# Kernel tuning notes

Measured on AMD Instinct MI355X. Metric: run time of the kernel, lower is better.

## Reference

```python
import jax, jax.numpy as jnp
import numpy as np

NUM_AGENT = 200
LOOK_BACK = 10
NUM_CTRL = 9
DIM = 512
HEADS = 8
DIM_HEAD = 64
N = NUM_AGENT * LOOK_BACK + NUM_CTRL  # 2009
BATCH = 4
SCALE = DIM_HEAD ** -0.5


def _build_mask():
    # eye(num_agent) repeat_interleaved by look_back on rows and cols == kron with ones(lb,lb)
    m = jnp.kron(jnp.eye(NUM_AGENT, dtype=jnp.float32),
                 jnp.ones((LOOK_BACK, LOOK_BACK), jnp.float32))
    # pad with zeros for the control-feature rows/cols
    return jnp.pad(m, ((0, NUM_CTRL), (0, NUM_CTRL)))  # [N, N]


def _split_heads(t):
    b, n, hd = t.shape
    return t.reshape(b, n, HEADS, hd // HEADS).transpose(0, 2, 1, 3)  # [b,h,n,d]


def setup_inputs() -> dict:
    key = jax.random.key(0)
    ks = jax.random.split(key, 5)
    inner = HEADS * DIM_HEAD
    return {
        "x": jax.random.normal(ks[0], (BATCH, N, DIM), jnp.float32),
        "w_qkv": jax.random.normal(ks[1], (DIM, inner * 3), jnp.float32) * 0.02,
        "w_qk_self": jax.random.normal(ks[2], (DIM, inner * 2), jnp.float32) * 0.02,
        "w_out": jax.random.normal(ks[3], (inner, DIM), jnp.float32) * 0.02,
        "b_out": jnp.zeros((DIM,), jnp.float32),
    }


def reference(x, w_qkv, w_qk_self, w_out, b_out):
    mask = _build_mask()  # [N, N], broadcasts over [b, h]
    q, k, v = map(_split_heads, jnp.split(x @ w_qkv, 3, axis=-1))
    q_s, k_s = map(_split_heads, jnp.split(x @ w_qk_self, 2, axis=-1))
    dots = jnp.einsum('bhnd,bhmd->bhnm', q, k) * SCALE
    dots_self = jnp.einsum('bhnd,bhmd->bhnm', q_s, k_s) * SCALE
    blended = mask * dots_self + (1.0 - mask) * dots
    attn = jax.nn.softmax(blended, axis=-1)  # [b,h,n,n]
    out = jnp.einsum('bhnm,bhmd->bhnd', attn, v)
    out = out.transpose(0, 2, 1, 3).reshape(x.shape[0], N, HEADS * DIM_HEAD)
    return out @ w_out + b_out, attn
```

## Files before the change

### kernel.cpp

```cpp
#include <hip/hip_runtime.h>
#include <hip/hip_bf16.h>


#define N_TOK   2009
#define NPAD    2048
#define NTILES  16
#define NT2     32
#define BATCH_  4
#define HEADS_  8
#define MROWS   8036
#define SCALE_  0.125f
#define RPB_A   256
#define RPV     64
#define PFP     68

typedef __attribute__((ext_vector_type(8)))  short sh8;
typedef __attribute__((ext_vector_type(16))) float f32x16;

static inline int cdiv(int a, int b) { return (a + b - 1) / b; }

__device__ __forceinline__ float4 ld4(const float* p) {
    return *reinterpret_cast<const float4*>(p);
}
__device__ __forceinline__ unsigned short f2bf(float f) {
    __hip_bfloat16 h = __float2bfloat16(f);
    return *reinterpret_cast<unsigned short*>(&h);
}
__device__ __forceinline__ float bf2f(unsigned short u) {
    return __uint_as_float(((unsigned)u) << 16);
}
__device__ __forceinline__ void cvt8(const float4& a, const float4& b, sh8& hi, sh8& lo) {
    float f[8] = {a.x, a.y, a.z, a.w, b.x, b.y, b.z, b.w};
#pragma unroll
    for (int i = 0; i < 8; ++i) {
        unsigned short h = f2bf(f[i]);
        hi[i] = (short)h;
        lo[i] = (short)f2bf(f[i] - bf2f(h));
    }
}
__device__ __forceinline__ void cvt8p(const float4& a, const float4& b, sh8& hi) {
#pragma unroll
    for (int i = 0; i < 4; ++i) {
        hi[i]     = (short)f2bf((&a.x)[i]);
        hi[4 + i] = (short)f2bf((&b.x)[i]);
    }
}
typedef const __attribute__((address_space(1))) void gas_void;
typedef __attribute__((address_space(3))) void las_void;
__device__ __forceinline__ void gll16(const void* g, void* l) {
    __builtin_amdgcn_global_load_lds((gas_void*)g, (las_void*)l, 16, 0, 0);
}

__device__ __forceinline__ void bar_lds() {
    asm volatile("s_waitcnt lgkmcnt(0)" ::: "memory");
    __builtin_amdgcn_sched_barrier(0);
    __builtin_amdgcn_s_barrier();
    __builtin_amdgcn_sched_barrier(0);
}
__device__ __forceinline__ void bar_keep16() {
    asm volatile("s_waitcnt vmcnt(16) lgkmcnt(0)" ::: "memory");
    __builtin_amdgcn_sched_barrier(0);
    __builtin_amdgcn_s_barrier();
    __builtin_amdgcn_sched_barrier(0);
}

__global__ __launch_bounds__(256)
void convert_x(const float* __restrict__ x, unsigned short* __restrict__ xh,
               unsigned short* __restrict__ xl)
{
    const int mt = blockIdx.x;
    const int yq = blockIdx.y;
    const int w  = threadIdx.x >> 6;
    const int kc = threadIdx.x & 63;
    for (int it = 0; it < 2; ++it) {
        int rg = (yq * 2 + it) * 4 + w;
        sh8 hi[4], lo[4];
#pragma unroll
        for (int rr = 0; rr < 4; ++rr) {
            int row = rg * 4 + rr;
            int gm = mt * 128 + row;
            int b = gm >> 11, gr = gm & 2047;
            float4 a = make_float4(0.f, 0.f, 0.f, 0.f), c = a;
            if (gr < N_TOK) {
                const float* p = x + ((size_t)b * N_TOK + gr) * 512 + kc * 8;
                a = ld4(p); c = ld4(p + 4);
            }
            cvt8(a, c, hi[rr], lo[rr]);
        }
        size_t base = ((size_t)(mt * 64 + kc) * 128 + rg * 4) * 8;
#pragma unroll
        for (int rr = 0; rr < 4; ++rr) {
            *reinterpret_cast<sh8*>(xh + base + rr * 8) = hi[rr];
            *reinterpret_cast<sh8*>(xl + base + rr * 8) = lo[rr];
        }
    }
}

__global__ __launch_bounds__(256)
void convert_w(const float* __restrict__ wqkv, const float* __restrict__ wself,
               const float* __restrict__ wout,
               unsigned short* __restrict__ qh, unsigned short* __restrict__ ql,
               unsigned short* __restrict__ sh, unsigned short* __restrict__ sl,
               unsigned short* __restrict__ oh, unsigned short* __restrict__ ol)
{
    int cid = blockIdx.x * 256 + threadIdx.x;
    int nt_all = cid >> 13, rem = cid & 8191;
    int kc = rem >> 7, col = rem & 127;
    const float* src; unsigned short *dh, *dl; int Nn, ntl;
    if (nt_all < 12)      { src = wqkv;  dh = qh; dl = ql; Nn = 1536; ntl = nt_all; }
    else if (nt_all < 20) { src = wself; dh = sh; dl = sl; Nn = 1024; ntl = nt_all - 12; }
    else                  { src = wout;  dh = oh; dl = ol; Nn = 512;  ntl = nt_all - 20; }
    float f[8];
#pragma unroll
    for (int i = 0; i < 8; ++i)
        f[i] = src[(size_t)(kc * 8 + i) * Nn + ntl * 128 + col];
    sh8 hi, lo;
    cvt8(make_float4(f[0], f[1], f[2], f[3]), make_float4(f[4], f[5], f[6], f[7]), hi, lo);
    size_t off = ((size_t)(ntl * 64 + kc) * 128 + col) * 8;
    *reinterpret_cast<sh8*>(dh + off) = hi;
    *reinterpret_cast<sh8*>(dl + off) = lo;
}

template<int MODE>
__global__ __launch_bounds__(512)
void gemm_bf16(const unsigned short* __restrict__ Ah, const unsigned short* __restrict__ Al,
               const unsigned short* __restrict__ Bh, const unsigned short* __restrict__ Bl,
               float* __restrict__ C, const float* __restrict__ bias)
{
    __shared__ __align__(16) unsigned short AhS[2][4096], AlS[2][4096],
                                            BhS[2][4096], BlS[2][4096];
    const int tid = threadIdx.x, lane = tid & 63, wid = tid >> 6;
    const int mt = blockIdx.x, ntile = blockIdx.y;
    const int wm = wid >> 2, wn = wid & 3;
    const int lj = lane & 31, g = lane >> 5;

    const unsigned short* Asrc_h = Ah + (size_t)mt * 65536;
    const unsigned short* Asrc_l = Al + (size_t)mt * 65536;
    const unsigned short* Bsrc_h = Bh + (size_t)ntile * 65536;
    const unsigned short* Bsrc_l = Bl + (size_t)ntile * 65536;

#define GSTAGE(BUF, S) do {                                                      \
    gll16(Asrc_h + (size_t)(S) * 4096 + tid * 8, (char*)AhS[BUF] + tid * 16);    \
    gll16(Asrc_l + (size_t)(S) * 4096 + tid * 8, (char*)AlS[BUF] + tid * 16);    \
    gll16(Bsrc_h + (size_t)(S) * 4096 + tid * 8, (char*)BhS[BUF] + tid * 16);    \
    gll16(Bsrc_l + (size_t)(S) * 4096 + tid * 8, (char*)BlS[BUF] + tid * 16);    \
} while (0)

    f32x16 acc[2];
#pragma unroll
    for (int i = 0; i < 16; ++i) { acc[0][i] = 0.f; acc[1][i] = 0.f; }

    GSTAGE(0, 0);
    for (int s = 0; s < 16; ++s) {
        const int buf = s & 1;
        __syncthreads();
        if (s + 1 < 16) GSTAGE(buf ^ 1, s + 1);
#pragma unroll
        for (int ks = 0; ks < 2; ++ks) {
            const int kcl = 2 * ks + g;
            sh8 bh = *reinterpret_cast<const sh8*>(BhS[buf] + (kcl * 128 + wn * 32 + lj) * 8);
            sh8 bl = *reinterpret_cast<const sh8*>(BlS[buf] + (kcl * 128 + wn * 32 + lj) * 8);
#pragma unroll
            for (int Mt = 0; Mt < 2; ++Mt) {
                sh8 ah = *reinterpret_cast<const sh8*>(AhS[buf] + (kcl * 128 + wm * 64 + Mt * 32 + lj) * 8);
                sh8 al = *reinterpret_cast<const sh8*>(AlS[buf] + (kcl * 128 + wm * 64 + Mt * 32 + lj) * 8);
                acc[Mt] = __builtin_amdgcn_mfma_f32_32x32x16_bf16(ah, bh, acc[Mt], 0, 0, 0);
                acc[Mt] = __builtin_amdgcn_mfma_f32_32x32x16_bf16(ah, bl, acc[Mt], 0, 0, 0);
                acc[Mt] = __builtin_amdgcn_mfma_f32_32x32x16_bf16(al, bh, acc[Mt], 0, 0, 0);
            }
        }
    }
#undef GSTAGE

#pragma unroll
    for (int Mt = 0; Mt < 2; ++Mt) {
#pragma unroll
        for (int reg = 0; reg < 16; ++reg) {
            int rloc = wm * 64 + Mt * 32 + (reg & 3) + 8 * (reg >> 2) + 4 * g;
            int gm = mt * 128 + rloc;
            int b = gm >> 11, gr = gm & 2047;
            if (gr < N_TOK) {
                int coln = ntile * 128 + wn * 32 + lj;
                float v = acc[Mt][reg];
                size_t idx;
                if (MODE == 1)
                    idx = ((size_t)(coln >> 9) * MROWS + (size_t)b * N_TOK + gr) * 512 + (coln & 511);
                else if (MODE == 0)
                    idx = ((size_t)b * N_TOK + gr) * 1024 + coln;
                else {
                    v += bias[coln];
                    idx = ((size_t)b * N_TOK + gr) * 512 + coln;
                }
                C[idx] = v;
            }
        }
    }
}

__global__ __launch_bounds__(256)
void selfE_k(const float* __restrict__ proj2, float* __restrict__ selfE)
{
    __shared__ float qs[10][64];
    __shared__ float ks[10][68];
    const int a = blockIdx.x;
    const int h = blockIdx.y & 7;
    const int b = blockIdx.y >> 3;
    const size_t rowbase = (size_t)b * N_TOK + a * 10;

    for (int i = threadIdx.x; i < 320; i += 256) {
        int r = i >> 4;
        int c = (i & 15) * 4;
        const float* src = proj2 + (rowbase + (r % 10)) * 1024
                         + (r < 10 ? 0 : 512) + h * 64 + c;
        float4 v = ld4(src);
        if (r < 10) *reinterpret_cast<float4*>(&qs[r][c]) = v;
        else        *reinterpret_cast<float4*>(&ks[r - 10][c]) = v;
    }
    __syncthreads();
    if (threadIdx.x < 100) {
        int r = threadIdx.x / 10, c = threadIdx.x % 10;
        float acc = 0.f;
#pragma unroll 8
        for (int d = 0; d < 64; ++d) acc += qs[r][d] * ks[c][d];
        int bh = b * HEADS_ + h;
        selfE[((size_t)bh * 2000 + a * 10 + r) * 10 + c] = __expf(acc * SCALE_);
    }
}

__global__ __launch_bounds__(256)
void convert_kv(const float* __restrict__ Kf, const float* __restrict__ Vf,
                unsigned short* __restrict__ Khg, unsigned short* __restrict__ Klg,
                unsigned short* __restrict__ Vtg)
{
    __shared__ float vtile[128][66];
    const int t  = blockIdx.x;
    const int h  = blockIdx.y & 7;
    const int b  = blockIdx.y >> 3;
    const int bh = blockIdx.y;
    const size_t bN = (size_t)b * N_TOK;
    const size_t tbase = ((size_t)bh * NTILES + t) * 8192;
    const int tid = threadIdx.x;

    {
        int r = tid >> 1, q = tid & 1;
        int gj = t * 128 + r;
        float4 f[8];
        if (gj < N_TOK) {
            const float* kp = Kf + (bN + gj) * 512 + h * 64 + q * 32;
#pragma unroll
            for (int i = 0; i < 8; ++i) f[i] = ld4(kp + 4 * i);
        } else {
#pragma unroll
            for (int i = 0; i < 8; ++i) f[i] = make_float4(0.f, 0.f, 0.f, 0.f);
        }
#pragma unroll
        for (int cp = 0; cp < 4; ++cp) {
            sh8 hi, lo;
            cvt8(f[2 * cp], f[2 * cp + 1], hi, lo);
            int kc = q * 4 + cp;
            size_t off = tbase + ((size_t)kc * 128 + r) * 8;
            *reinterpret_cast<sh8*>(Khg + off) = hi;
            *reinterpret_cast<sh8*>(Klg + off) = lo;
        }
    }
    {
        int r = tid >> 1, q = tid & 1;
        int gj = t * 128 + r;
        const float* vp = Vf + (bN + gj) * 512 + h * 64 + q * 32;
#pragma unroll
        for (int i = 0; i < 8; ++i) {
            float4 v = (gj < N_TOK) ? ld4(vp + 4 * i) : make_float4(0.f, 0.f, 0.f, 0.f);
            *reinterpret_cast<float4*>(&vtile[r][q * 32 + 4 * i]) = v;
        }
    }
    __syncthreads();
    {
        int d = tid & 63, jg = tid >> 6;
#pragma unroll
        for (int jj = 0; jj < 4; ++jj) {
            int jc = jg * 4 + jj;
            sh8 pk;
#pragma unroll
            for (int i = 0; i < 8; ++i) pk[i] = (short)f2bf(vtile[jc * 8 + i][d]);
            *reinterpret_cast<sh8*>(Vtg + tbase + ((size_t)jc * 64 + d) * 8) = pk;
        }
    }
}

__global__ __launch_bounds__(512, 2)
void attn_rowsum(const float* __restrict__ Qf,
                 const unsigned short* __restrict__ Khg,
                 const float* __restrict__ selfE,
                 float* __restrict__ rowinv)
{
    __shared__ __align__(16) unsigned short KhS[2][8192];
    __shared__ float selfS[RPB_A * 10];

    const int bid = blockIdx.x;
    const int xcd = bid & 7, idx = bid >> 3;
    const int bh  = xcd * 4 + (idx >> 3);
    const int bx  = idx & 7;
    const int h = bh & 7, b = bh >> 3;
    const int tid = threadIdx.x, lane = tid & 63, wid = tid >> 6;
    const int row0 = bx * RPB_A;
    const int wr = wid * 32;
    const size_t bN = (size_t)b * N_TOK;
    const int lj = lane & 31, g = lane >> 5;

    for (int i = tid; i < RPB_A * 10; i += 512) {
        int r = i / 10, c = i - r * 10;
        int gr = row0 + r;
        selfS[i] = (gr < 2000) ? selfE[((size_t)bh * 2000 + gr) * 10 + c] : 0.f;
    }

    sh8 qh[4];
    {
        int grow = row0 + wr + lj;
        bool val = grow < N_TOK;
        const float* qp = Qf + (bN + (val ? grow : 0)) * 512 + h * 64;
#pragma unroll
        for (int ks = 0; ks < 4; ++ks) {
            int kc = 2 * ks + g;
            float4 a = val ? ld4(qp + kc * 8)     : make_float4(0.f, 0.f, 0.f, 0.f);
            float4 c = val ? ld4(qp + kc * 8 + 4) : make_float4(0.f, 0.f, 0.f, 0.f);
            cvt8p(a, c, qh[ks]);
        }
    }

    const unsigned short* ktiles = Khg + (size_t)bh * NTILES * 8192;
#define RSTAGE(T) do {                                                          \
    const unsigned short* kt = ktiles + (size_t)(T) * 8192;                     \
    char* dst = (char*)KhS[(T) & 1];                                            \
    _Pragma("unroll") for (int i = 0; i < 2; ++i)                               \
        gll16(kt + i * 4096 + tid * 8, dst + i * 8192 + tid * 16); } while (0)

    RSTAGE(0);

    float rsacc[16];
#pragma unroll
    for (int i = 0; i < 16; ++i) rsacc[i] = 0.f;

    const int alo = (row0 / 10) * 10;
    const int rmax = row0 + RPB_A - 1 < 1999 ? row0 + RPB_A - 1 : 1999;
    const int ahi = (rmax / 10) * 10 + 10;

    for (int t = 0; t < NTILES; ++t) {
        __syncthreads();
        if (t + 1 < NTILES) RSTAGE(t + 1);
        const unsigned short* kb = KhS[t & 1];
        const bool dtile = (alo < t * 128 + 128) && (ahi > t * 128);
#pragma unroll
        for (int ct = 0; ct < 4; ++ct) {
            sh8 kf[4];
#pragma unroll
            for (int ks = 0; ks < 4; ++ks)
                kf[ks] = *reinterpret_cast<const sh8*>(kb + ((2 * ks + g) * 128 + 32 * ct + lj) * 8);
            f32x16 s;
#pragma unroll
            for (int i = 0; i < 16; ++i) s[i] = 0.f;
#pragma unroll
            for (int ks = 0; ks < 4; ++ks)
                s = __builtin_amdgcn_mfma_f32_32x32x16_bf16(qh[ks], kf[ks], s, 0, 0, 0);
            const int gj = t * 128 + 32 * ct + lj;
            if (gj < N_TOK) {
#pragma unroll
                for (int reg = 0; reg < 16; ++reg) {
                    int rloc = wr + (reg & 3) + 8 * (reg >> 2) + 4 * g;
                    int grow = row0 + rloc;
                    float e = __expf(s[reg] * SCALE_);
                    if (dtile && grow < 2000) {
                        int a0 = (grow / 10) * 10;
                        unsigned cc = (unsigned)(gj - a0);
                        if (cc < 10u) e = selfS[rloc * 10 + (int)cc];
                    }
                    rsacc[reg] += e;
                }
            }
        }
    }
#undef RSTAGE

#pragma unroll
    for (int reg = 0; reg < 16; ++reg) {
        float v = rsacc[reg];
        v += __shfl_xor(v, 1);  v += __shfl_xor(v, 2);
        v += __shfl_xor(v, 4);  v += __shfl_xor(v, 8);
        v += __shfl_xor(v, 16);
        rsacc[reg] = v;
    }
    if (lj == 0) {
#pragma unroll
        for (int reg = 0; reg < 16; ++reg) {
            int rloc = wr + (reg & 3) + 8 * (reg >> 2) + 4 * g;
            int grow = row0 + rloc;
            rowinv[(size_t)bh * NPAD + row0 + rloc] =
                (grow < N_TOK) ? 1.0f / rsacc[reg] : 0.f;
        }
    }
}

__global__ __launch_bounds__(256, 3)
void attn_pv(const float* __restrict__ Qf,
             const unsigned short* __restrict__ Khg,
             const unsigned short* __restrict__ Klg,
             const unsigned short* __restrict__ Vtg,
             const float* __restrict__ selfE,
             const float* __restrict__ rowinv,
             float* __restrict__ attn,
             unsigned short* __restrict__ Ohg, unsigned short* __restrict__ Olg,
             float* __restrict__ dump)
{
    extern __shared__ __align__(16) char smem[];
    unsigned short* KhS = (unsigned short*)smem;
    unsigned short* KlS = KhS + 4096;
    unsigned short* VtS = KlS + 4096;
    float* Pf = (float*)(VtS + 8192);
    unsigned short* selfS = (unsigned short*)(Pf + RPV * PFP);
    float* rinvS = (float*)(selfS + RPV * 10);

    const int bid = blockIdx.x;
    const int xcd = bid & 7, sub = bid >> 3;
    const int bh  = xcd * 4 + (sub >> 5);
    const int bx  = sub & 31;
    const int h = bh & 7, b = bh >> 3;
    const int tid = threadIdx.x, lane = tid & 63, wid = tid >> 6;
    const int row0 = bx * RPV;
    const int wr = (wid & 1) * 32;
    const int cw = wid >> 1;
    const size_t bN = (size_t)b * N_TOK;
    const size_t abase = ((size_t)bh * N_TOK + row0) * N_TOK;
    const int lj = lane & 31, g = lane >> 5;
    float* dumpT = dump + ((size_t)bid << 6) + lane;

    for (int i = tid; i < RPV * 10; i += 256) {
        int r = i / 10, c = i - r * 10;
        int gr = row0 + r;
        selfS[i] = (gr < 2000) ? f2bf(selfE[((size_t)bh * 2000 + gr) * 10 + c]) : 0;
    }
    if (tid < RPV) rinvS[tid] = rowinv[(size_t)bh * NPAD + row0 + tid];

    sh8 qh[4], ql[4];
    {
        int grow = row0 + wr + lj;
        bool val = grow < N_TOK;
        const float* qp = Qf + (bN + (val ? grow : 0)) * 512 + h * 64;
#pragma unroll
        for (int ks = 0; ks < 4; ++ks) {
            int kc = 2 * ks + g;
            float4 a = val ? ld4(qp + kc * 8)     : make_float4(0.f, 0.f, 0.f, 0.f);
            float4 c = val ? ld4(qp + kc * 8 + 4) : make_float4(0.f, 0.f, 0.f, 0.f);
            cvt8(a, c, qh[ks], ql[ks]);
        }
    }

    const unsigned short* khT = Khg + (size_t)bh * NTILES * 8192;
    const unsigned short* klT = Klg + (size_t)bh * NTILES * 8192;
    const unsigned short* vtT = Vtg + (size_t)bh * NTILES * 8192;

#define STAGE_KH(T) do { const unsigned short* src = khT + (size_t)((T) >> 1) * 8192 \
        + 512 * ((T) & 1);                                                           \
    _Pragma("unroll") for (int r_ = 0; r_ < 2; ++r_) {                               \
        int s_ = tid + 256 * r_;                                                     \
        gll16(src + ((s_ >> 6) * 1024 + (s_ & 63) * 8), (char*)KhS + s_ * 16);       \
    } } while (0)
#define STAGE_KL(T) do { const unsigned short* src = klT + (size_t)((T) >> 1) * 8192 \
        + 512 * ((T) & 1);                                                           \
    _Pragma("unroll") for (int r_ = 0; r_ < 2; ++r_) {                               \
        int s_ = tid + 256 * r_;                                                     \
        gll16(src + ((s_ >> 6) * 1024 + (s_ & 63) * 8), (char*)KlS + s_ * 16);       \
    } } while (0)
#define STAGE_VT(T) do { const unsigned short* src = vtT + (size_t)((T) >> 1) * 8192 \
        + 4096 * ((T) & 1);                                                          \
    char* dst = (char*)VtS + ((T) & 1) * 8192;                                       \
    _Pragma("unroll") for (int r_ = 0; r_ < 2; ++r_) {                               \
        int s_ = tid + 256 * r_;                                                     \
        gll16(src + s_ * 8, dst + s_ * 16);                                          \
    } } while (0)

#define QK_PHASE(T) do {                                                            \
        const bool dtile = (alo < (T) * 64 + 64) && (ahi > (T) * 64);               \
        sh8 kfh[4], kfl[4];                                                         \
        _Pragma("unroll") for (int ks = 0; ks < 4; ++ks) {                          \
            int off = ((2 * ks + g) * 64 + 32 * cw + lj) * 8;                       \
            kfh[ks] = *reinterpret_cast<const sh8*>(KhS + off);                     \
            kfl[ks] = *reinterpret_cast<const sh8*>(KlS + off);                     \
        }                                                                           \
        f32x16 s;                                                                   \
        _Pragma("unroll") for (int i = 0; i < 16; ++i) s[i] = 0.f;                  \
        _Pragma("unroll") for (int ks = 0; ks < 4; ++ks) {                          \
            s = __builtin_amdgcn_mfma_f32_32x32x16_bf16(qh[ks], kfh[ks], s, 0,0,0); \
            s = __builtin_amdgcn_mfma_f32_32x32x16_bf16(qh[ks], kfl[ks], s, 0,0,0); \
            s = __builtin_amdgcn_mfma_f32_32x32x16_bf16(ql[ks], kfh[ks], s, 0,0,0); \
        }                                                                           \
        const int cin = 32 * cw + lj;                                               \
        const int gj  = (T) * 64 + cin;                                             \
        const bool jv = gj < N_TOK;                                                 \
        _Pragma("unroll") for (int reg = 0; reg < 16; ++reg) {                      \
            int rowl = (reg & 3) + 8 * (reg >> 2) + 4 * g;                          \
            int rloc = wr + rowl;                                                   \
            int grow = row0 + rloc;                                                 \
            float e = 0.f;                                                          \
            if (jv && grow < N_TOK) e = __expf(s[reg] * SCALE_);                    \
            if (dtile && jv && grow < 2000) {                                       \
                int a0 = (grow / 10) * 10;                                          \
                unsigned cc = (unsigned)(gj - a0);                                  \
                if (cc < 10u) e = bf2f(selfS[rloc * 10 + (int)cc]);                 \
            }                                                                       \
            Pf[rloc * PFP + cin] = e * rinvS[rloc];                                 \
        }                                                                           \
    } while (0)

#define PV_PHASE(T) do {                                                            \
        const unsigned short* vtb = VtS + ((T) & 1) * 4096;                         \
        _Pragma("unroll") for (int m = 0; m < 4; ++m) {                             \
            const float* pp = &Pf[(wr + lj) * PFP + 16 * m + 8 * g];                \
            float4 a = ld4(pp), b4 = ld4(pp + 4);                                   \
            sh8 pa; cvt8p(a, b4, pa);                                               \
            sh8 vf = *reinterpret_cast<const sh8*>(                                 \
                vtb + ((2 * m + g) * 64 + 32 * cw + lj) * 8);                       \
            oacc = __builtin_amdgcn_mfma_f32_32x32x16_bf16(pa, vf, oacc, 0, 0, 0);  \
        }                                                                           \
    } while (0)

    STAGE_KH(0); STAGE_KL(0); STAGE_VT(0);

    const int alo = (row0 / 10) * 10;
    const int rmax = row0 + RPV - 1 < 1999 ? row0 + RPV - 1 : 1999;
    const int ahi = (rmax / 10) * 10 + 10;

    f32x16 oacc;
#pragma unroll
    for (int i = 0; i < 16; ++i) oacc[i] = 0.f;

    __syncthreads();

    const int rbase = wid * 16;

    for (int t = 0; t < NT2 - 1; ++t) {
        QK_PHASE(t);
        bar_lds();
        STAGE_KH(t + 1); STAGE_KL(t + 1); STAGE_VT(t + 1);
        {
            float* ap0 = attn + abase + (size_t)t * 64 + lane;
#pragma unroll
            for (int i = 0; i < 16; ++i) {
                int r = rbase + i;
                int grow = row0 + r;
                float v = Pf[r * PFP + lane];
                float* sdst = (grow < N_TOK) ? (ap0 + (size_t)r * N_TOK) : dumpT;
                *sdst = v;
            }
        }
        PV_PHASE(t);
        bar_keep16();
    }

    {
        const int t = NT2 - 1;
        QK_PHASE(t);
        __syncthreads();
        PV_PHASE(t);
        if (t * 64 + lane < N_TOK) {
            float* ap0 = attn + abase + (size_t)t * 64 + lane;
#pragma unroll
            for (int i = 0; i < 16; ++i) {
                int r = rbase + i;
                int grow = row0 + r;
                if (grow < N_TOK)
                    ap0[(size_t)r * N_TOK] = Pf[r * PFP + lane];
            }
        }
        __syncthreads();
    }
#undef STAGE_KH
#undef STAGE_KL
#undef STAGE_VT
#undef QK_PHASE
#undef PV_PHASE

    float* Ofull = (float*)smem;
#pragma unroll
    for (int reg = 0; reg < 16; ++reg) {
        int rloc = wr + (reg & 3) + 8 * (reg >> 2) + 4 * g;
        Ofull[rloc * 68 + 32 * cw + lj] = oacc[reg];
    }
    __syncthreads();
#pragma unroll
    for (int it = 0; it < 2; ++it) {
        int task = it * 256 + tid;
        int row = task >> 3, kq = task & 7;
        const float* op = Ofull + row * 68 + kq * 8;
        float4 a = ld4(op), c = ld4(op + 4);
        sh8 hi, lo; cvt8(a, c, hi, lo);
        int gm = b * 2048 + row0 + row;
        int mtile = gm >> 7, row128 = gm & 127;
        size_t off = ((size_t)(mtile * 64 + h * 8 + kq) * 128 + row128) * 8;
        *reinterpret_cast<sh8*>(Ohg + off) = hi;
        *reinterpret_cast<sh8*>(Olg + off) = lo;
    }
}

extern "C" void kernel_launch(void* const* d_in, const int* in_sizes, int n_in,
                              void* d_out, int out_size, void* d_ws, size_t ws_size,
                              hipStream_t stream)
{
    const float* x         = (const float*)d_in[0];
    const float* w_qkv     = (const float*)d_in[1];
    const float* w_qk_self = (const float*)d_in[2];
    const float* w_out     = (const float*)d_in[3];
    const float* b_out     = (const float*)d_in[4];

    float* out  = (float*)d_out;
    float* attn = out + (size_t)MROWS * 512;

    float* Qf = (float*)d_ws;
    float* Kf = Qf + (size_t)MROWS * 512;
    float* Vf = Kf + (size_t)MROWS * 512;
    float* p2 = Vf + (size_t)MROWS * 512;
    unsigned short* Khg = (unsigned short*)p2;
    unsigned short* Klg = Khg + 4194304;
    unsigned short* Vtg = Klg + 4194304;
    float* proj2 = p2;
    float* after_p2 = p2 + (size_t)MROWS * 1024;
    unsigned short* xh  = (unsigned short*)after_p2;
    unsigned short* xl  = xh + 4194304;
    unsigned short* Wqh = xl + 4194304;
    unsigned short* Wql = Wqh + 786432;
    unsigned short* Wsh = Wql + 786432;
    unsigned short* Wsl = Wsh + 524288;
    unsigned short* Woh = Wsl + 524288;
    unsigned short* Wol = Woh + 262144;
    float* rowinv = (float*)(Wol + 262144);
    float* selfE  = rowinv + 65536;
    float* dump   = selfE + 640000;
    unsigned short* Ohg = (unsigned short*)Kf;
    unsigned short* Olg = Ohg + 4194304;

    const int smem_pv = 8192 + 8192 + 16384
                      + RPV * PFP * 4
                      + RPV * 10 * 2 + RPV * 4;
    hipFuncSetAttribute((const void*)attn_pv,
                        hipFuncAttributeMaxDynamicSharedMemorySize, smem_pv);

    dim3 gx(64, 4);
    convert_x<<<gx, 256, 0, stream>>>(x, xh, xl);
    convert_w<<<768, 256, 0, stream>>>(w_qkv, w_qk_self, w_out,
                                       Wqh, Wql, Wsh, Wsl, Woh, Wol);

    dim3 g1(64, 12);
    gemm_bf16<1><<<g1, 512, 0, stream>>>(xh, xl, Wqh, Wql, Qf, nullptr);

    dim3 g2(64, 8);
    gemm_bf16<0><<<g2, 512, 0, stream>>>(xh, xl, Wsh, Wsl, proj2, nullptr);

    dim3 gs(200, 32);
    selfE_k<<<gs, 256, 0, stream>>>(proj2, selfE);

    dim3 gc(NTILES, 32);
    convert_kv<<<gc, 256, 0, stream>>>(Kf, Vf, Khg, Klg, Vtg);

    attn_rowsum<<<256, 512, 0, stream>>>(Qf, Khg, selfE, rowinv);

    attn_pv<<<1024, 256, smem_pv, stream>>>(Qf, Khg, Klg, Vtg, selfE, rowinv,
                                            attn, Ohg, Olg, dump);

    dim3 g3(64, 4);
    gemm_bf16<2><<<g3, 512, 0, stream>>>(Ohg, Olg, Woh, Wol, out, b_out);
}
```

Measured before the change: 510.4 us.

## Specialize attn_pv warps into compute and attention-store producer groups

Doubles the attn_pv block to 512 threads. Four waves run the QK/PV MFMA loop and four dedicated waves stream the normalized probability tile from LDS to the global attn output, synchronized by block barriers. The goal is to take the large attn matrix store off the compute waves' critical path. In exchange it adds two full barriers per tile, drains vmcnt(0) after every tile instead of keeping loads in flight, and raises register and occupancy pressure under launch_bounds(512,4).

```diff
diff --git a/kernel.cpp b/kernel.cpp
--- a/kernel.cpp
+++ b/kernel.cpp
@@ -49,19 +49,6 @@
 typedef __attribute__((address_space(3))) void las_void;
 __device__ __forceinline__ void gll16(const void* g, void* l) {
     __builtin_amdgcn_global_load_lds((gas_void*)g, (las_void*)l, 16, 0, 0);
-}
-
-__device__ __forceinline__ void bar_lds() {
-    asm volatile("s_waitcnt lgkmcnt(0)" ::: "memory");
-    __builtin_amdgcn_sched_barrier(0);
-    __builtin_amdgcn_s_barrier();
-    __builtin_amdgcn_sched_barrier(0);
-}
-__device__ __forceinline__ void bar_keep16() {
-    asm volatile("s_waitcnt vmcnt(16) lgkmcnt(0)" ::: "memory");
-    __builtin_amdgcn_sched_barrier(0);
-    __builtin_amdgcn_s_barrier();
-    __builtin_amdgcn_sched_barrier(0);
 }
 
 __global__ __launch_bounds__(256)
@@ -399,7 +386,7 @@
     }
 }
 
-__global__ __launch_bounds__(256, 3)
+__global__ __launch_bounds__(512, 4)
 void attn_pv(const float* __restrict__ Qf,
              const unsigned short* __restrict__ Khg,
              const unsigned short* __restrict__ Klg,
@@ -407,8 +394,7 @@
              const float* __restrict__ selfE,
              const float* __restrict__ rowinv,
              float* __restrict__ attn,
-             unsigned short* __restrict__ Ohg, unsigned short* __restrict__ Olg,
-             float* __restrict__ dump)
+             unsigned short* __restrict__ Ohg, unsigned short* __restrict__ Olg)
 {
     extern __shared__ __align__(16) char smem[];
     unsigned short* KhS = (unsigned short*)smem;
@@ -425,14 +411,14 @@
     const int h = bh & 7, b = bh >> 3;
     const int tid = threadIdx.x, lane = tid & 63, wid = tid >> 6;
     const int row0 = bx * RPV;
-    const int wr = (wid & 1) * 32;
-    const int cw = wid >> 1;
     const size_t bN = (size_t)b * N_TOK;
     const size_t abase = ((size_t)bh * N_TOK + row0) * N_TOK;
     const int lj = lane & 31, g = lane >> 5;
-    float* dumpT = dump + ((size_t)bid << 6) + lane;
-
-    for (int i = tid; i < RPV * 10; i += 256) {
+    const bool is_compute = (wid < 4);
+    const int wr = (wid & 1) * 32;
+    const int cw = (wid >> 1) & 1;
+
+    for (int i = tid; i < RPV * 10; i += 512) {
         int r = i / 10, c = i - r * 10;
         int gr = row0 + r;
         selfS[i] = (gr < 2000) ? f2bf(selfE[((size_t)bh * 2000 + gr) * 10 + c]) : 0;
@@ -440,7 +426,7 @@
     if (tid < RPV) rinvS[tid] = rowinv[(size_t)bh * NPAD + row0 + tid];
 
     sh8 qh[4], ql[4];
-    {
+    if (is_compute) {
         int grow = row0 + wr + lj;
         bool val = grow < N_TOK;
         const float* qp = Qf + (bN + (val ? grow : 0)) * 512 + h * 64;
@@ -522,8 +508,6 @@
         }                                                                           \
     } while (0)
 
-    STAGE_KH(0); STAGE_KL(0); STAGE_VT(0);
-
     const int alo = (row0 / 10) * 10;
     const int rmax = row0 + RPV - 1 < 1999 ? row0 + RPV - 1 : 1999;
     const int ahi = (rmax / 10) * 10 + 10;
@@ -532,45 +516,53 @@
 #pragma unroll
     for (int i = 0; i < 16; ++i) oacc[i] = 0.f;
 
-    __syncthreads();
-
-    const int rbase = wid * 16;
-
-    for (int t = 0; t < NT2 - 1; ++t) {
-        QK_PHASE(t);
-        bar_lds();
-        STAGE_KH(t + 1); STAGE_KL(t + 1); STAGE_VT(t + 1);
-        {
-            float* ap0 = attn + abase + (size_t)t * 64 + lane;
-#pragma unroll
-            for (int i = 0; i < 16; ++i) {
-                int r = rbase + i;
-                int grow = row0 + r;
-                float v = Pf[r * PFP + lane];
-                float* sdst = (grow < N_TOK) ? (ap0 + (size_t)r * N_TOK) : dumpT;
-                *sdst = v;
+    if (is_compute) {
+        STAGE_KH(0); STAGE_KL(0); STAGE_VT(0);
+        asm volatile("s_waitcnt vmcnt(0) lgkmcnt(0)" ::: "memory");
+        __builtin_amdgcn_sched_barrier(0);
+        __builtin_amdgcn_s_barrier();
+        __builtin_amdgcn_sched_barrier(0);
+        for (int t = 0; t < NT2; ++t) {
+            QK_PHASE(t);
+            asm volatile("s_waitcnt lgkmcnt(0)" ::: "memory");
+            __builtin_amdgcn_sched_barrier(0);
+            __builtin_amdgcn_s_barrier();
+            __builtin_amdgcn_sched_barrier(0);
+            if (t + 1 < NT2) { STAGE_KH(t + 1); STAGE_KL(t + 1); STAGE_VT(t + 1); }
+            PV_PHASE(t);
+            asm volatile("s_waitcnt vmcnt(0) lgkmcnt(0)" ::: "memory");
+            __builtin_amdgcn_sched_barrier(0);
+            __builtin_amdgcn_s_barrier();
+            __builtin_amdgcn_sched_barrier(0);
+        }
+    } else {
+        const int sw = wid - 4;
+        asm volatile("s_waitcnt lgkmcnt(0)" ::: "memory");
+        __builtin_amdgcn_sched_barrier(0);
+        __builtin_amdgcn_s_barrier();
+        __builtin_amdgcn_sched_barrier(0);
+        for (int t = 0; t < NT2; ++t) {
+            asm volatile("s_waitcnt lgkmcnt(0)" ::: "memory");
+            __builtin_amdgcn_sched_barrier(0);
+            __builtin_amdgcn_s_barrier();
+            __builtin_amdgcn_sched_barrier(0);
+            {
+                const int gj = t * 64 + lane;
+                const bool colv = gj < N_TOK;
+                float* ap0 = attn + abase + gj;
+#pragma unroll
+                for (int i = 0; i < 16; ++i) {
+                    int r = sw * 16 + i;
+                    float v = Pf[r * PFP + lane];
+                    if (colv && (row0 + r) < N_TOK)
+                        ap0[(size_t)r * N_TOK] = v;
+                }
             }
-        }
-        PV_PHASE(t);
-        bar_keep16();
-    }
-
-    {
-        const int t = NT2 - 1;
-        QK_PHASE(t);
-        __syncthreads();
-        PV_PHASE(t);
-        if (t * 64 + lane < N_TOK) {
-            float* ap0 = attn + abase + (size_t)t * 64 + lane;
-#pragma unroll
-            for (int i = 0; i < 16; ++i) {
-                int r = rbase + i;
-                int grow = row0 + r;
-                if (grow < N_TOK)
-                    ap0[(size_t)r * N_TOK] = Pf[r * PFP + lane];
-            }
-        }
-        __syncthreads();
+            asm volatile("s_waitcnt lgkmcnt(0)" ::: "memory");
+            __builtin_amdgcn_sched_barrier(0);
+            __builtin_amdgcn_s_barrier();
+            __builtin_amdgcn_sched_barrier(0);
+        }
     }
 #undef STAGE_KH
 #undef STAGE_KL
@@ -578,16 +570,18 @@
 #undef QK_PHASE
 #undef PV_PHASE
 
+    __syncthreads();
     float* Ofull = (float*)smem;
-#pragma unroll
-    for (int reg = 0; reg < 16; ++reg) {
-        int rloc = wr + (reg & 3) + 8 * (reg >> 2) + 4 * g;
-        Ofull[rloc * 68 + 32 * cw + lj] = oacc[reg];
+    if (is_compute) {
+#pragma unroll
+        for (int reg = 0; reg < 16; ++reg) {
+            int rloc = wr + (reg & 3) + 8 * (reg >> 2) + 4 * g;
+            Ofull[rloc * 68 + 32 * cw + lj] = oacc[reg];
+        }
     }
     __syncthreads();
-#pragma unroll
-    for (int it = 0; it < 2; ++it) {
-        int task = it * 256 + tid;
+    {
+        int task = tid;
         int row = task >> 3, kq = task & 7;
         const float* op = Ofull + row * 68 + kq * 8;
         float4 a = ld4(op), c = ld4(op + 4);
@@ -632,7 +626,6 @@
     unsigned short* Wol = Woh + 262144;
     float* rowinv = (float*)(Wol + 262144);
     float* selfE  = rowinv + 65536;
-    float* dump   = selfE + 640000;
     unsigned short* Ohg = (unsigned short*)Kf;
     unsigned short* Olg = Ohg + 4194304;
 
@@ -661,8 +654,8 @@
 
     attn_rowsum<<<256, 512, 0, stream>>>(Qf, Khg, selfE, rowinv);
 
-    attn_pv<<<1024, 256, smem_pv, stream>>>(Qf, Khg, Klg, Vtg, selfE, rowinv,
-                                            attn, Ohg, Olg, dump);
+    attn_pv<<<1024, 512, smem_pv, stream>>>(Qf, Khg, Klg, Vtg, selfE, rowinv,
+                                            attn, Ohg, Olg);
 
     dim3 g3(64, 4);
     gemm_bf16<2><<<g3, 512, 0, stream>>>(Ohg, Olg, Woh, Wol, out, b_out);
```

Result: faster. 490.5 us (-3.9%).
